# Kernel optimization log

Hardware: AMD Instinct MI355X
Metric: run time of the kernel (lower is better)

Reference implementation:

```python
import jax, jax.numpy as jnp
import numpy as np

# static module hyperparameters (match init_kwargs)
DIMS = 1024
HEAD = 16
HD = DIMS // HEAD          # 64
MAX_ITER = 3
MIN_SIZE = 64
MAX_SIZE = 2048
UP_WIN, DOWN_WIN = 1.1, 0.9
UP_DIFF, DOWN_DIFF = 0.05, 0.001
B, T = 2, 1024


def _ln(x, w, eps=1e-5):
    # torch LayerNorm with bias=False (weight only), biased variance
    m = jnp.mean(x, axis=-1, keepdims=True)
    v = jnp.var(x, axis=-1, keepdims=True)
    return (x - m) * jax.lax.rsqrt(v + eps) * w


def setup_inputs() -> dict:
    key = jax.random.key(0)
    ks = jax.random.split(key, 12)

    def lin_w(k, o, i):
        return (jax.random.normal(k, (o, i), dtype=jnp.float32) / np.sqrt(i)).astype(jnp.float32)

    return {
        "x": jax.random.normal(ks[0], (B, T, DIMS), dtype=jnp.float32),
        "Wq": lin_w(ks[1], DIMS, DIMS), "bq": jnp.zeros((DIMS,), jnp.float32),
        "Wk": lin_w(ks[2], DIMS, DIMS),
        "Wv": lin_w(ks[3], DIMS, DIMS), "bv": jnp.zeros((DIMS,), jnp.float32),
        "Wo": lin_w(ks[4], DIMS, DIMS), "bo": jnp.zeros((DIMS,), jnp.float32),
        "lna_w": jnp.ones((DIMS,), jnp.float32),
        "lnb_w": jnp.ones((DIMS,), jnp.float32),
        "lnc_w": jnp.ones((HD,), jnp.float32),
        "lnd_w": jnp.ones((HD,), jnp.float32),
        "lq_w": lin_w(ks[5], HD, HD), "lq_b": jnp.zeros((HD,), jnp.float32),
        "lk_w": lin_w(ks[6], HD, HD), "lk_b": jnp.zeros((HD,), jnp.float32),
        "lv_w": lin_w(ks[7], HD, HD), "lv_b": jnp.zeros((HD,), jnp.float32),
        "threshold": jnp.float32(0.01),
        "temp_base": jnp.float32(1.0),
        "factor": jnp.float32(0.1),
    }


def _focus(x, Wq, bq, Wk, Wv, bv, Wo, bo, lna_w, lnb_w, lnc_w, lnd_w,
           lq_w, lq_b, lk_w, lk_b, lv_w, lv_b, threshold, temp_base, factor):
    b, t, d = x.shape
    q = _ln(x, lna_w) @ Wq.T + bq
    kk = _ln(x, lnb_w) @ Wk.T
    v = _ln(x, lnb_w) @ Wv.T + bv
    sc = HD ** (-0.25)

    def _shape(u):
        return u.reshape(b, t, HEAD, HD).transpose(0, 2, 1, 3)  # [B,H,T,hd]

    q_full = _shape(q * sc)
    k_full = _shape(kk * sc)
    v_full = _shape(v)

    # .item() calls in torch detach these from the graph
    thr = jax.lax.stop_gradient(threshold)
    fac = jax.lax.stop_gradient(factor)
    t0 = jax.lax.stop_gradient(temp_base)

    cw0 = jnp.int32(max(min(t, MAX_SIZE), MIN_SIZE))
    inv_sqrt_e = jnp.float32(1.0 / np.sqrt(HD))  # SDPA default scale
    pos = jnp.arange(t)

    def step(carry, i):
        qcur, prev, attn, cw, temp, done = carry
        # LocalOut projections over full length (out-of-window part masked below)
        qp = qcur @ lq_w.T + lq_b
        kp = k_full @ lk_w.T + lk_b
        vp = v_full @ lv_w.T + lv_b
        sq = _ln(qp, lnc_w)
        sk = _ln(kp, lnd_w)
        tscale = jnp.where(temp > 0, jax.lax.rsqrt(temp), jnp.float32(1.0))
        sq = sq * tscale
        scores = jnp.einsum('bhqd,bhkd->bhqk', sq, sk) * inv_sqrt_e
        in_win = pos < cw
        scores = jnp.where(in_win[None, None, None, :], scores, -jnp.inf)
        probs = jax.nn.softmax(scores, axis=-1)
        out = jnp.einsum('bhqk,bhkd->bhqd', probs, vp)
        # rows >= cur_win stay zero (iter_out buffer semantics)
        iter_out = jnp.where(in_win[None, None, :, None], out, 0.0)

        diff = jnp.mean(jnp.abs(iter_out - prev))
        converged = (diff < thr + fac * diff) & (i > 0)
        upd = (~done) & (~converged)            # continue iterating
        new_done = done | converged

        attn_n = jnp.where(done, attn, iter_out)
        prev_n = jnp.where(upd, iter_out, prev)
        qcur_n = jnp.where(upd, qcur + iter_out, qcur)
        # _next_win
        up = (cw.astype(jnp.float32) * UP_WIN).astype(jnp.int32)
        down = (cw.astype(jnp.float32) * DOWN_WIN).astype(jnp.int32)
        nw = jnp.where(diff > UP_DIFF, up,
                       jnp.where((diff < DOWN_DIFF) & (cw > MIN_SIZE), down, cw))
        nw = jnp.clip(nw, MIN_SIZE, t)
        cw_n = jnp.where(upd, nw, cw)
        temp_n = jnp.where(upd, temp + jnp.float32(0.005), temp)
        return (qcur_n, prev_n, attn_n, cw_n, temp_n, new_done), None

    zeros = jnp.zeros_like(q_full)
    carry0 = (q_full, zeros, zeros, cw0, t0, jnp.array(False))
    (_, _, attn_out, _, _, _), _ = jax.lax.scan(step, carry0, jnp.arange(MAX_ITER))

    output = attn_out.transpose(0, 2, 1, 3).reshape(b, t, d)
    return output @ Wo.T + bo


def reference(x, Wq, bq, Wk, Wv, bv, Wo, bo, lna_w, lnb_w, lnc_w, lnd_w,
              lq_w, lq_b, lk_w, lk_b, lv_w, lv_b, threshold, temp_base, factor):
    return _focus(x, Wq, bq, Wk, Wv, bv, Wo, bo, lna_w, lnb_w, lnc_w, lnd_w,
                  lq_w, lq_b, lk_w, lk_b, lv_w, lv_b, threshold, temp_base, factor)
```

## Files before the change

### kernel.cpp

```cpp
#include <hip/hip_runtime.h>
#include <hip/hip_bf16.h>

#define BDIM 2
#define TDIM 1024
#define DDIM 1024
#define HDIM 16
#define HD   64
#define RROWS (BDIM * TDIM)
#define BH    (BDIM * HDIM)
#define NHE   (BH * TDIM * HD)
#define NHE4  (NHE / 4)
#define DIFF_BLOCKS 512
#define L2E 1.4426950408889634f

typedef __attribute__((ext_vector_type(8))) short short8v;
typedef __attribute__((ext_vector_type(4))) short short4v;
typedef __attribute__((ext_vector_type(8))) _Float16 half8v;
typedef __attribute__((ext_vector_type(4))) _Float16 half4v;
typedef __attribute__((ext_vector_type(4))) float f32x4;

struct FState {
  int   cw;
  float temp;
  int   done;
  int   upd;
  int   done_prev;
  float thr;
  float fac;
  int   pad;
};

static __device__ __forceinline__ unsigned short f2bf(float x) {
  __hip_bfloat16 h = __float2bfloat16(x);
  return __builtin_bit_cast(unsigned short, h);
}
static __device__ __forceinline__ void gload16(const void* g, void* l) {
  __builtin_amdgcn_global_load_lds(
      (const __attribute__((address_space(1))) void*)g,
      (__attribute__((address_space(3))) void*)l, 16, 0, 0);
}

__global__ void init_kernel(FState* st, const float* thr, const float* tb, const float* fac) {
  if (threadIdx.x == 0 && blockIdx.x == 0) {
    st->cw = TDIM;
    st->temp = tb[0];
    st->done = 0;
    st->done_prev = 0;
    st->upd = 1;
    st->thr = thr[0];
    st->fac = fac[0];
  }
}

__global__ __launch_bounds__(256) void ln_x_kernel(
    const float* __restrict__ x, const float* __restrict__ wa, const float* __restrict__ wb,
    _Float16* __restrict__ xaH, _Float16* __restrict__ xbH)
{
  const int row = blockIdx.x;
  const int tid = threadIdx.x;
  const float4 v = reinterpret_cast<const float4*>(x + (size_t)row * DDIM)[tid];
  float s = v.x + v.y + v.z + v.w;
  float q = v.x * v.x + v.y * v.y + v.z * v.z + v.w * v.w;
#pragma unroll
  for (int off = 1; off < 64; off <<= 1) {
    s += __shfl_xor(s, off);
    q += __shfl_xor(q, off);
  }
  __shared__ float ss[4], qq[4];
  const int lane = tid & 63, wv = tid >> 6;
  if (lane == 0) { ss[wv] = s; qq[wv] = q; }
  __syncthreads();
  s = ss[0] + ss[1] + ss[2] + ss[3];
  q = qq[0] + qq[1] + qq[2] + qq[3];
  const float mean = s * (1.0f / DDIM);
  const float var  = q * (1.0f / DDIM) - mean * mean;
  const float inv  = rsqrtf(var + 1e-5f);
  const float4 a4 = reinterpret_cast<const float4*>(wa)[tid];
  const float4 b4 = reinterpret_cast<const float4*>(wb)[tid];
  const float hv[4] = { (v.x - mean) * inv, (v.y - mean) * inv,
                        (v.z - mean) * inv, (v.w - mean) * inv };
  const float av[4] = { a4.x, a4.y, a4.z, a4.w };
  const float bv[4] = { b4.x, b4.y, b4.z, b4.w };
  half4v ha, hb;
#pragma unroll
  for (int j = 0; j < 4; ++j) {
    ha[j] = (_Float16)(hv[j] * av[j]);
    hb[j] = (_Float16)(hv[j] * bv[j]);
  }
  *reinterpret_cast<half4v*>(xaH + (size_t)row * DDIM + tid * 4) = ha;
  *reinterpret_cast<half4v*>(xbH + (size_t)row * DDIM + tid * 4) = hb;
}

__global__ __launch_bounds__(256) void w_cvt_kernel(
    const float* __restrict__ W0, const float* __restrict__ W1,
    const float* __restrict__ W2, const float* __restrict__ W3,
    const float* __restrict__ W4,
    _Float16* __restrict__ O0, _Float16* __restrict__ O1,
    _Float16* __restrict__ O2, _Float16* __restrict__ O3,
    _Float16* __restrict__ O4)
{
  const float* W; _Float16* O;
  switch (blockIdx.y) {
    case 0:  W = W0; O = O0; break;
    case 1:  W = W1; O = O1; break;
    case 2:  W = W2; O = O2; break;
    case 3:  W = W3; O = O3; break;
    default:
      if (blockIdx.x >= 4) return;
      W = W4; O = O4; break;
  }
  const int r = blockIdx.x;
  const int tid = threadIdx.x;
  const float4 v = reinterpret_cast<const float4*>(W + (size_t)r * 1024)[tid];
  half4v h;
  h[0] = (_Float16)v.x; h[1] = (_Float16)v.y;
  h[2] = (_Float16)v.z; h[3] = (_Float16)v.w;
  *reinterpret_cast<half4v*>(O + (size_t)r * 1024 + tid * 4) = h;
}

template<int CMODE>
__global__ __launch_bounds__(256) void gemm_mfma_kernel(
    const _Float16* __restrict__ A0, const _Float16* __restrict__ W0,
    const float* __restrict__ b0, float* __restrict__ C0, float s0,
    const _Float16* __restrict__ A1, const _Float16* __restrict__ W1,
    const float* __restrict__ b1, float* __restrict__ C1, float s1,
    const _Float16* __restrict__ A2, const _Float16* __restrict__ W2,
    const float* __restrict__ b2, float* __restrict__ C2, float s2)
{
  const _Float16* A; const _Float16* W; const float* bias; float* C; float scale;
  switch (blockIdx.z) {
    case 0:  A = A0; W = W0; bias = b0; C = C0; scale = s0; break;
    case 1:  A = A1; W = W1; bias = b1; C = C1; scale = s1; break;
    default: A = A2; W = W2; bias = b2; C = C2; scale = s2; break;
  }
  __shared__ __align__(16) _Float16 As[128 * 32];
  __shared__ __align__(16) _Float16 Ws[128 * 32];
  const int tid = threadIdx.x;
  const int wv = tid >> 6, lane = tid & 63;
  const int wm = wv >> 1, wn = wv & 1;
  const int bm = blockIdx.x;
  const int bn = blockIdx.y;

  const _Float16* gA[2]; const _Float16* gW[2];
  _Float16* lA[2]; _Float16* lW[2];
#pragma unroll
  for (int j = 0; j < 2; ++j) {
    const int chunk = wv * 2 + j;
    const int r = chunk * 16 + (lane >> 2);
    const int ce = (lane & 3) * 8;
    gA[j] = A + (size_t)(bm * 128 + r) * 1024 + ce;
    gW[j] = W + (size_t)(bn * 128 + r) * 1024 + ce;
    lA[j] = As + chunk * 512;
    lW[j] = Ws + chunk * 512;
  }

  f32x4 acc[4][4] = {};
  const int rb = lane & 15;
  const int kb = (lane >> 4) * 8;

  for (int ks = 0; ks < 1024; ks += 32) {
    __syncthreads();
#pragma unroll
    for (int j = 0; j < 2; ++j) {
      gload16(gA[j] + ks, lA[j]);
      gload16(gW[j] + ks, lW[j]);
    }
    __syncthreads();
    half8v af[4], wf[4];
#pragma unroll
    for (int f = 0; f < 4; ++f) {
      af[f] = *reinterpret_cast<const half8v*>(As + (wm * 64 + f * 16 + rb) * 32 + kb);
      wf[f] = *reinterpret_cast<const half8v*>(Ws + (wn * 64 + f * 16 + rb) * 32 + kb);
    }
#pragma unroll
    for (int i = 0; i < 4; ++i)
#pragma unroll
      for (int j2 = 0; j2 < 4; ++j2)
        acc[i][j2] = __builtin_amdgcn_mfma_f32_16x16x32_f16(af[i], wf[j2], acc[i][j2], 0, 0, 0);
  }

#pragma unroll
  for (int j2 = 0; j2 < 4; ++j2) {
    const int n = bn * 128 + wn * 64 + j2 * 16 + (lane & 15);
    const float bv_ = bias ? bias[n] : 0.0f;
#pragma unroll
    for (int i = 0; i < 4; ++i) {
#pragma unroll
      for (int r = 0; r < 4; ++r) {
        const int m = bm * 128 + wm * 64 + i * 16 + (lane >> 4) * 4 + r;
        const float v = (acc[i][j2][r] + bv_) * scale;
        size_t ci;
        if constexpr (CMODE == 0) {
          ci = (size_t)m * 1024 + n;
        } else {
          const int b = m >> 10, t = m & (TDIM - 1);
          ci = ((size_t)(b * HDIM + (n >> 6)) * TDIM + t) * HD + (n & 63);
        }
        C[ci] = v;
      }
    }
  }
}

template<int OUT_MODE, bool DO_LN>
static __device__ __forceinline__ void headproj_body(
    const float* __restrict__ in, unsigned short* __restrict__ out,
    const float* __restrict__ w, const float* __restrict__ bias,
    const float* __restrict__ lnw, float* wl, unsigned short* tT)
{
  const int tid = threadIdx.x;
  for (int idx = tid; idx < 4096; idx += 256) {
    const int d = idx >> 6, i = idx & 63;
    wl[i * 65 + d] = w[idx];
  }
  const int lane = tid & 63, wv = tid >> 6;
  const float bd = bias[lane];
  float lw = 1.0f;
  if constexpr (DO_LN) lw = lnw[lane];
  __syncthreads();
  const int rowBase = blockIdx.x * 32 + wv * 8;
  for (int rr = 0; rr < 8; ++rr) {
    const int row = rowBase + rr;
    const float h = in[(size_t)row * HD + lane];
    float y = bd;
#pragma unroll
    for (int i = 0; i < 64; ++i) {
      const float hv = __uint_as_float((unsigned)__builtin_amdgcn_readlane((int)__float_as_uint(h), i));
      y += wl[i * 65 + lane] * hv;
    }
    if constexpr (DO_LN) {
      float s = y;
#pragma unroll
      for (int off = 1; off < 64; off <<= 1) s += __shfl_xor(s, off);
      const float mean = s * (1.0f / 64.0f);
      const float t0 = y - mean;
      float v2 = t0 * t0;
#pragma unroll
      for (int off = 1; off < 64; off <<= 1) v2 += __shfl_xor(v2, off);
      y = t0 * rsqrtf(v2 * (1.0f / 64.0f) + 1e-5f) * lw;
    }
    if constexpr (OUT_MODE == 0) {
      out[(size_t)row * HD + lane] = f2bf(y);
    } else {
      tT[lane * 34 + wv * 8 + rr] = f2bf(y);
    }
  }
  if constexpr (OUT_MODE == 1) {
    __syncthreads();
    const int hd = tid >> 2, tseg = (tid & 3) * 8;
    const int r0 = blockIdx.x * 32;
    const int bh = r0 >> 10, t0 = r0 & (TDIM - 1);
    short8v v;
#pragma unroll
    for (int i = 0; i < 8; ++i) v[i] = (short)tT[hd * 34 + tseg + i];
    *reinterpret_cast<short8v*>(out + ((size_t)bh * HD + hd) * TDIM + t0 + tseg) = v;
  }
}

__global__ __launch_bounds__(256) void headproj_kv_kernel(
    const float* __restrict__ kin, unsigned short* __restrict__ skb,
    const float* __restrict__ lkw, const float* __restrict__ lkb,
    const float* __restrict__ lnd,
    const float* __restrict__ vin, unsigned short* __restrict__ vpT,
    const float* __restrict__ lvw, const float* __restrict__ lvb)
{
  __shared__ float wl[64 * 65];
  __shared__ unsigned short tT[64 * 34];
  if (blockIdx.y == 0)
    headproj_body<0, true >(kin, skb, lkw, lkb, lnd, wl, tT);
  else
    headproj_body<1, false>(vin, vpT, lvw, lvb, (const float*)nullptr, wl, tT);
}

__global__ __launch_bounds__(512) void attn_mfma_kernel(
    const float* __restrict__ qcur, const unsigned short* __restrict__ sk,
    const unsigned short* __restrict__ vpT, float* __restrict__ io,
    const float* __restrict__ prev, _Float16* __restrict__ attnH,
    const _Float16* __restrict__ lqwH, const float* __restrict__ lqb,
    const float* __restrict__ lnc, float* __restrict__ partials,
    const FState* __restrict__ st, int is_first)
{
  if (st->done) return;
  const int lid = blockIdx.x;
  const int xcd = lid & 7;
  const int rr_ = lid >> 3;
  const int qb  = rr_ & 15;
  const int bh  = (rr_ >> 4) * 8 + xcd;

  const int cw = st->cw;
  const int tid = threadIdx.x;
  const int wv = tid >> 6, lane = tid & 63;
  const int wq = wv & 3, wk = wv >> 2;
  const int ql = lane & 15, hi = lane >> 4;
  const int qbase = qb * 64 + wq * 16;
  const int q = qbase + ql;
  const size_t baseRow = (size_t)bh * TDIM * HD;
  const size_t baseT   = (size_t)bh * HD * TDIM;
  float* orow = io + baseRow + (size_t)q * HD;
  const float* prow = prev + baseRow + (size_t)q * HD;
  float* qcrow = const_cast<float*>(qcur) + baseRow + (size_t)q * HD;
  const bool wvalid = (qbase < cw);
  _Float16* arow = attnH + (size_t)((bh >> 4) * TDIM + q) * 1024 + (bh & 15) * HD;

  __shared__ __align__(16) unsigned char KV[2][2][2][8192];
  __shared__ __align__(16) unsigned char PJ[8][2048];
  float* wred = reinterpret_cast<float*>(&KV[1][1][0][0]);

  const int sub  = lane >> 3;
  const int colB = (lane & 7) * 16;
  const int scol = (colB ^ (sub << 4)) >> 1;

  const int kb0 = wk * 512;
  const unsigned short* kSrc0 = sk  + baseRow + (size_t)(kb0 + wq * 16 + sub) * HD + scol;
  const unsigned short* vSrc0 = vpT + baseT  + (size_t)(wq * 16 + sub) * TDIM + scol;

  unsigned char* pj = (unsigned char*)PJ[wv];
  const unsigned swz8 = (unsigned)((ql & 7) << 4);

  const int nch0 = (min(cw, 512) + 63) >> 6;
  const int nch1 = (cw > 512) ? ((cw - 512 + 63) >> 6) : 0;
  const int nchOwn = wk ? nch1 : nch0;

  if (nchOwn > 0) {
#pragma unroll
    for (int jj = 0; jj < 2; ++jj) {
      gload16(kSrc0 + (size_t)(jj * 8) * HD, &KV[wk][0][0][(wq * 2 + jj) * 1024]);
      gload16(vSrc0 + (size_t)(jj * 8) * TDIM + kb0, &KV[wk][0][1][(wq * 2 + jj) * 1024]);
    }
  }

  short8v qf0, qf1;
  if (wvalid) {
    const float tp = st->temp;
    const float ts = (tp > 0.0f ? rsqrtf(tp) : 1.0f) * 0.125f;
    half8v qh0, qh1;
    {
      const f32x4 a0 = *reinterpret_cast<const f32x4*>(qcrow + hi * 8);
      const f32x4 a1 = *reinterpret_cast<const f32x4*>(qcrow + hi * 8 + 4);
      const f32x4 b0 = *reinterpret_cast<const f32x4*>(qcrow + 32 + hi * 8);
      const f32x4 b1 = *reinterpret_cast<const f32x4*>(qcrow + 32 + hi * 8 + 4);
#pragma unroll
      for (int j = 0; j < 4; ++j) {
        qh0[j] = (_Float16)a0[j]; qh0[4 + j] = (_Float16)a1[j];
        qh1[j] = (_Float16)b0[j]; qh1[4 + j] = (_Float16)b1[j];
      }
    }
    f32x4 sp[4];
#pragma unroll
    for (int f = 0; f < 4; ++f) {
      const half8v a0 = *reinterpret_cast<const half8v*>(lqwH + (f * 16 + ql) * 64 + hi * 8);
      const half8v a1 = *reinterpret_cast<const half8v*>(lqwH + (f * 16 + ql) * 64 + 32 + hi * 8);
      f32x4 acc = {};
      acc = __builtin_amdgcn_mfma_f32_16x16x32_f16(a0, qh0, acc, 0, 0, 0);
      acc = __builtin_amdgcn_mfma_f32_16x16x32_f16(a1, qh1, acc, 0, 0, 0);
      sp[f] = acc;
    }
    float sum = 0.f;
#pragma unroll
    for (int f = 0; f < 4; ++f) {
      const f32x4 b4 = *reinterpret_cast<const f32x4*>(lqb + f * 16 + hi * 4);
      sp[f] += b4;
      sum += (sp[f][0] + sp[f][1]) + (sp[f][2] + sp[f][3]);
    }
    sum += __shfl_xor(sum, 16);
    sum += __shfl_xor(sum, 32);
    const float mean = sum * (1.0f / 64.0f);
    float vs = 0.f;
#pragma unroll
    for (int f = 0; f < 4; ++f) {
#pragma unroll
      for (int r = 0; r < 4; ++r) {
        const float t0 = sp[f][r] - mean;
        sp[f][r] = t0;
        vs += t0 * t0;
      }
    }
    vs += __shfl_xor(vs, 16);
    vs += __shfl_xor(vs, 32);
    const float inv = rsqrtf(vs * (1.0f / 64.0f) + 1e-5f);
    const unsigned wb = (unsigned)(ql * 128 + hi * 8);
#pragma unroll
    for (int f = 0; f < 4; ++f) {
      const f32x4 lc = *reinterpret_cast<const f32x4*>(lnc + f * 16 + hi * 4);
      const float y0 = sp[f][0] * inv * lc[0] * ts;
      const float y1 = sp[f][1] * inv * lc[1] * ts;
      const float y2 = sp[f][2] * inv * lc[2] * ts;
      const float y3 = sp[f][3] * inv * lc[3] * ts;
      *reinterpret_cast<unsigned*>(pj + ((wb + f * 32)     ^ swz8)) =
          (unsigned)f2bf(y0) | ((unsigned)f2bf(y1) << 16);
      *reinterpret_cast<unsigned*>(pj + ((wb + f * 32 + 4) ^ swz8)) =
          (unsigned)f2bf(y2) | ((unsigned)f2bf(y3) << 16);
    }
    qf0 = *reinterpret_cast<short8v*>(pj + ((unsigned)(ql * 128 + hi * 16) ^ swz8));
    qf1 = *reinterpret_cast<short8v*>(pj + ((unsigned)(ql * 128 + 64 + hi * 16) ^ swz8));
  }
  __syncthreads();

  float m = -1e30f, l = 0.f;
  f32x4 o[4] = {};
  int cur = 0;
  for (int ch = 0; ch < nch0; ++ch) {
    if (ch + 1 < nchOwn) {
      const size_t kn = (size_t)(ch + 1) * 64;
#pragma unroll
      for (int jj = 0; jj < 2; ++jj) {
        gload16(kSrc0 + (kn + (size_t)(jj * 8)) * HD, &KV[wk][cur ^ 1][0][(wq * 2 + jj) * 1024]);
        gload16(vSrc0 + (size_t)(jj * 8) * TDIM + kb0 + kn, &KV[wk][cur ^ 1][1][(wq * 2 + jj) * 1024]);
      }
    }
    if (wvalid && ch < nchOwn) {
      const int k0 = kb0 + ch * 64;
      const unsigned char* kt = &KV[wk][cur][0][0];
      const unsigned char* vt = &KV[wk][cur][1][0];
      f32x4 s[4];
#pragma unroll
      for (int f = 0; f < 4; ++f) {
        const unsigned rb = (unsigned)((f * 16 + ql) * 128);
        const short8v a0 = *reinterpret_cast<const short8v*>(kt + rb + ((unsigned)(hi * 16) ^ swz8));
        const short8v a1 = *reinterpret_cast<const short8v*>(kt + rb + ((unsigned)(64 + hi * 16) ^ swz8));
        f32x4 acc = {};
        acc = __builtin_amdgcn_mfma_f32_16x16x32_bf16(a0, qf0, acc, 0, 0, 0);
        acc = __builtin_amdgcn_mfma_f32_16x16x32_bf16(a1, qf1, acc, 0, 0, 0);
        s[f] = acc;
      }
      float mc = -1e30f;
      if (k0 + 64 > cw) {
#pragma unroll
        for (int f = 0; f < 4; ++f)
#pragma unroll
          for (int r = 0; r < 4; ++r) {
            float v = s[f][r];
            if (k0 + f * 16 + hi * 4 + r >= cw) v = -1e30f;
            s[f][r] = v;
            mc = fmaxf(mc, v);
          }
      } else {
#pragma unroll
        for (int f = 0; f < 4; ++f)
#pragma unroll
          for (int r = 0; r < 4; ++r) mc = fmaxf(mc, s[f][r]);
      }
      mc = fmaxf(mc, __shfl_xor(mc, 16));
      mc = fmaxf(mc, __shfl_xor(mc, 32));
      if (__any(mc > m + 8.0f)) {
        const float mn = fmaxf(m, mc);
        const float c = __builtin_amdgcn_exp2f((m - mn) * L2E);
        l *= c;
#pragma unroll
        for (int f = 0; f < 4; ++f) o[f] *= c;
        m = mn;
      }
      float ls = 0.f;
      unsigned pk[8];
#pragma unroll
      for (int f = 0; f < 4; ++f) {
        const float p0 = __builtin_amdgcn_exp2f((s[f][0] - m) * L2E);
        const float p1 = __builtin_amdgcn_exp2f((s[f][1] - m) * L2E);
        const float p2 = __builtin_amdgcn_exp2f((s[f][2] - m) * L2E);
        const float p3 = __builtin_amdgcn_exp2f((s[f][3] - m) * L2E);
        ls += (p0 + p1) + (p2 + p3);
        pk[f * 2]     = (unsigned)f2bf(p0) | ((unsigned)f2bf(p1) << 16);
        pk[f * 2 + 1] = (unsigned)f2bf(p2) | ((unsigned)f2bf(p3) << 16);
      }
      ls += __shfl_xor(ls, 16);
      ls += __shfl_xor(ls, 32);
      l += ls;
      const unsigned wb = (unsigned)(ql * 128 + hi * 8);
#pragma unroll
      for (int f = 0; f < 4; ++f) {
        *reinterpret_cast<unsigned*>(pj + ((wb + f * 32)     ^ swz8)) = pk[f * 2];
        *reinterpret_cast<unsigned*>(pj + ((wb + f * 32 + 4) ^ swz8)) = pk[f * 2 + 1];
      }
#pragma unroll
      for (int kh = 0; kh < 2; ++kh) {
        const short8v pb = *reinterpret_cast<short8v*>(
            pj + ((unsigned)(ql * 128 + kh * 64 + hi * 16) ^ swz8));
#pragma unroll
        for (int f = 0; f < 4; ++f) {
          const unsigned rb = (unsigned)((f * 16 + ql) * 128);
          const short8v av = *reinterpret_cast<const short8v*>(
              vt + rb + ((unsigned)(kh * 64 + hi * 16) ^ swz8));
          o[f] = __builtin_amdgcn_mfma_f32_16x16x32_bf16(av, pb, o[f], 0, 0, 0);
        }
      }
    }
    __syncthreads();
    cur ^= 1;
  }

  float* Obuf = reinterpret_cast<float*>(&KV[0][0][0][0]);
  if (wk == 1 && wvalid) {
    if (hi == 0) {
      Obuf[4352 + wq * 16 + ql] = m;
      Obuf[4416 + wq * 16 + ql] = l;
    }
#pragma unroll
    for (int f = 0; f < 4; ++f)
      *reinterpret_cast<f32x4*>(&Obuf[(wq * 16 + ql) * 68 + f * 16 + hi * 4]) = o[f];
  }
  __syncthreads();

  float pd = 0.0f;
  if (wk == 0) {
    if (wvalid) {
      const float m1 = Obuf[4352 + wq * 16 + ql];
      const float l1 = Obuf[4416 + wq * 16 + ql];
      const float mn = fmaxf(m, m1);
      const float c0 = __builtin_amdgcn_exp2f((m - mn) * L2E);
      const float c1 = __builtin_amdgcn_exp2f((m1 - mn) * L2E);
      const float lt = l * c0 + l1 * c1;
      const bool valid = (q < cw);
      const float invl = valid ? (1.0f / lt) : 0.0f;
#pragma unroll
      for (int f = 0; f < 4; ++f) {
        const f32x4 o1 = *reinterpret_cast<const f32x4*>(&Obuf[(wq * 16 + ql) * 68 + f * 16 + hi * 4]);
        const f32x4 vo = (o[f] * c0 + o1 * c1) * invl;
        *reinterpret_cast<f32x4*>(orow + f * 16 + hi * 4) = vo;
        half4v h4;
        h4[0] = (_Float16)vo[0]; h4[1] = (_Float16)vo[1];
        h4[2] = (_Float16)vo[2]; h4[3] = (_Float16)vo[3];
        *reinterpret_cast<half4v*>(arow + f * 16 + hi * 4) = h4;
        const f32x4 qv = *reinterpret_cast<const f32x4*>(qcrow + f * 16 + hi * 4);
        *reinterpret_cast<f32x4*>(qcrow + f * 16 + hi * 4) = qv + vo;
        if (!is_first) {
          const f32x4 pv = *reinterpret_cast<const f32x4*>(prow + f * 16 + hi * 4);
          pd += fabsf(vo[0] - pv[0]) + fabsf(vo[1] - pv[1]) +
                fabsf(vo[2] - pv[2]) + fabsf(vo[3] - pv[3]);
        } else {
          pd += fabsf(vo[0]) + fabsf(vo[1]) + fabsf(vo[2]) + fabsf(vo[3]);
        }
      }
    } else {
      const f32x4 z = {0.f, 0.f, 0.f, 0.f};
      const half4v hz = { (_Float16)0.f, (_Float16)0.f, (_Float16)0.f, (_Float16)0.f };
#pragma unroll
      for (int f = 0; f < 4; ++f) {
        *reinterpret_cast<f32x4*>(orow + f * 16 + hi * 4) = z;
        *reinterpret_cast<half4v*>(arow + f * 16 + hi * 4) = hz;
        if (!is_first) {
          const f32x4 pv = *reinterpret_cast<const f32x4*>(prow + f * 16 + hi * 4);
          pd += fabsf(pv[0]) + fabsf(pv[1]) + fabsf(pv[2]) + fabsf(pv[3]);
        }
      }
    }
  }

#pragma unroll
  for (int off = 1; off < 64; off <<= 1) pd += __shfl_xor(pd, off);
  if (lane == 0) wred[wv] = pd;
  __syncthreads();
  if (tid == 0)
    partials[lid] = wred[0] + wred[1] + wred[2] + wred[3] +
                    wred[4] + wred[5] + wred[6] + wred[7];
}

__global__ __launch_bounds__(256) void state_update_kernel(
    FState* __restrict__ st, const float* __restrict__ partials, int iter)
{
  const int tid = threadIdx.x;
  float s = 0.0f;
  for (int i = tid; i < DIFF_BLOCKS; i += 256) s += partials[i];
  __shared__ float red[256];
  red[tid] = s;
  __syncthreads();
  for (int off = 128; off > 0; off >>= 1) {
    if (tid < off) red[tid] += red[tid + off];
    __syncthreads();
  }
  if (tid == 0) {
    const int done_prev = st->done;
    st->done_prev = done_prev;
    if (!done_prev) {
      const float diff = red[0] * (1.0f / (float)NHE);
      const bool conv = (diff < st->thr + st->fac * diff) && (iter > 0);
      st->upd  = conv ? 0 : 1;
      st->done = conv ? 1 : 0;
      if (!conv) {
        const int cw = st->cw;
        const int up = (int)((float)cw * 1.1f);
        const int dn = (int)((float)cw * 0.9f);
        int nw = (diff > 0.05f) ? up : ((diff < 0.001f && cw > 64) ? dn : cw);
        nw = nw < 64 ? 64 : (nw > TDIM ? TDIM : nw);
        st->cw = nw;
        st->temp += 0.005f;
      }
    } else {
      st->upd = 0;
    }
  }
}

extern "C" void kernel_launch(void* const* d_in, const int* in_sizes, int n_in,
                              void* d_out, int out_size, void* d_ws, size_t ws_size,
                              hipStream_t stream)
{
  const float* x   = (const float*)d_in[0];
  const float* Wq  = (const float*)d_in[1];
  const float* bq  = (const float*)d_in[2];
  const float* Wk  = (const float*)d_in[3];
  const float* Wv  = (const float*)d_in[4];
  const float* bv  = (const float*)d_in[5];
  const float* Wo  = (const float*)d_in[6];
  const float* bo  = (const float*)d_in[7];
  const float* lna = (const float*)d_in[8];
  const float* lnb = (const float*)d_in[9];
  const float* lnc = (const float*)d_in[10];
  const float* lnd = (const float*)d_in[11];
  const float* lqw = (const float*)d_in[12];
  const float* lqb = (const float*)d_in[13];
  const float* lkw = (const float*)d_in[14];
  const float* lkb = (const float*)d_in[15];
  const float* lvw = (const float*)d_in[16];
  const float* lvb = (const float*)d_in[17];
  const float* thr = (const float*)d_in[18];
  const float* tb  = (const float*)d_in[19];
  const float* fac = (const float*)d_in[20];
  float* out = (float*)d_out;

  float* f0   = (float*)d_ws;
  float* qcur = f0;
  float* io0  = f0 + (size_t)NHE;
  float* io1  = f0 + 2 * (size_t)NHE;
  _Float16* h0   = (_Float16*)(f0 + 3 * (size_t)NHE);
  _Float16* xaH  = h0;
  _Float16* attnH = h0;
  _Float16* xbH  = h0 + (size_t)RROWS * 1024;
  _Float16* WqH  = xbH + (size_t)RROWS * 1024;
  _Float16* WkH  = WqH + (size_t)1048576;
  _Float16* WvH  = WkH + (size_t)1048576;
  _Float16* WoH  = WvH + (size_t)1048576;
  _Float16* lqwH = WoH + (size_t)1048576;
  unsigned short* skb = (unsigned short*)(lqwH + 4096);
  unsigned short* vpT = skb + (size_t)NHE;
  float* partials = (float*)(vpT + (size_t)NHE);
  FState* st = (FState*)(partials + DIFF_BLOCKS);

  constexpr float SC = 0.35355339059327379f;

  hipLaunchKernelGGL(init_kernel, dim3(1), dim3(64), 0, stream, st, thr, tb, fac);
  hipLaunchKernelGGL(ln_x_kernel, dim3(RROWS), dim3(256), 0, stream, x, lna, lnb, xaH, xbH);
  hipLaunchKernelGGL(w_cvt_kernel, dim3(1024, 5), dim3(256), 0, stream,
                     Wq, Wk, Wv, Wo, lqw, WqH, WkH, WvH, WoH, lqwH);

  hipLaunchKernelGGL((gemm_mfma_kernel<1>), dim3(16, 8, 3), dim3(256), 0, stream,
                     xaH, WqH, bq, qcur, SC,
                     xbH, WkH, (const float*)nullptr, io0, SC,
                     xbH, WvH, bv, io1, 1.0f);

  hipLaunchKernelGGL(headproj_kv_kernel, dim3(1024, 2), dim3(256), 0, stream,
                     io0, skb, lkw, lkb, lnd, io1, vpT, lvw, lvb);

  for (int it = 0; it < 3; ++it) {
    float* io   = (it & 1) ? io1 : io0;
    float* prev = (it & 1) ? io0 : io1;
    hipLaunchKernelGGL(attn_mfma_kernel, dim3(DIFF_BLOCKS), dim3(512), 0, stream,
                       qcur, skb, vpT, io, prev, attnH, lqwH, lqb, lnc,
                       partials, st, it == 0 ? 1 : 0);
    hipLaunchKernelGGL(state_update_kernel, dim3(1), dim3(256), 0, stream,
                       st, partials, it);
  }

  hipLaunchKernelGGL((gemm_mfma_kernel<0>), dim3(16, 8, 1), dim3(256), 0, stream,
                     attnH, WoH, bo, out, 1.0f,
                     attnH, WoH, bo, out, 1.0f,
                     attnH, WoH, bo, out, 1.0f);
}
```

Before: 161.3 us.

## Merge init, layernorm and weight-convert kernels; add MFMA priority hints

Folds the state-init, input layernorm and weight fp32-to-fp16 conversion kernels into a single prep kernel dispatched over a flat block range, removing two kernel launches. It also raises wave priority with s_setprio around the QK and PV MFMA sections of the attention kernel, and unrolls the partials reduction in the state-update kernel to a fixed two loads per thread. The merged grid puts branch divergence by block index into one kernel, and the priority hints may or may not help wave scheduling.

```diff
diff --git a/kernel.cpp b/kernel.cpp
--- a/kernel.cpp
+++ b/kernel.cpp
@@ -40,24 +40,56 @@
       (__attribute__((address_space(3))) void*)l, 16, 0, 0);
 }
 
-__global__ void init_kernel(FState* st, const float* thr, const float* tb, const float* fac) {
-  if (threadIdx.x == 0 && blockIdx.x == 0) {
-    st->cw = TDIM;
-    st->temp = tb[0];
-    st->done = 0;
-    st->done_prev = 0;
-    st->upd = 1;
-    st->thr = thr[0];
-    st->fac = fac[0];
-  }
-}
-
-__global__ __launch_bounds__(256) void ln_x_kernel(
+__global__ __launch_bounds__(256) void prep_kernel(
     const float* __restrict__ x, const float* __restrict__ wa, const float* __restrict__ wb,
-    _Float16* __restrict__ xaH, _Float16* __restrict__ xbH)
+    _Float16* __restrict__ xaH, _Float16* __restrict__ xbH,
+    const float* __restrict__ W0, const float* __restrict__ W1,
+    const float* __restrict__ W2, const float* __restrict__ W3,
+    const float* __restrict__ W4,
+    _Float16* __restrict__ O0, _Float16* __restrict__ O1,
+    _Float16* __restrict__ O2, _Float16* __restrict__ O3,
+    _Float16* __restrict__ O4,
+    FState* st, const float* thr, const float* tb, const float* fac)
 {
-  const int row = blockIdx.x;
+  const int bid = blockIdx.x;
   const int tid = threadIdx.x;
+
+  if (bid >= 6148) {
+    if (tid == 0) {
+      st->cw = TDIM;
+      st->temp = tb[0];
+      st->done = 0;
+      st->done_prev = 0;
+      st->upd = 1;
+      st->thr = thr[0];
+      st->fac = fac[0];
+    }
+    return;
+  }
+
+  if (bid >= 2048) {
+    const int idx = bid - 2048;
+    const float* W; _Float16* O; int r;
+    if (bid >= 6144) { W = W4; O = O4; r = bid - 6144; }
+    else {
+      const int mat = idx >> 10;
+      r = idx & 1023;
+      switch (mat) {
+        case 0:  W = W0; O = O0; break;
+        case 1:  W = W1; O = O1; break;
+        case 2:  W = W2; O = O2; break;
+        default: W = W3; O = O3; break;
+      }
+    }
+    const float4 v = reinterpret_cast<const float4*>(W + (size_t)r * 1024)[tid];
+    half4v h;
+    h[0] = (_Float16)v.x; h[1] = (_Float16)v.y;
+    h[2] = (_Float16)v.z; h[3] = (_Float16)v.w;
+    *reinterpret_cast<half4v*>(O + (size_t)r * 1024 + tid * 4) = h;
+    return;
+  }
+
+  const int row = bid;
   const float4 v = reinterpret_cast<const float4*>(x + (size_t)row * DDIM)[tid];
   float s = v.x + v.y + v.z + v.w;
   float q = v.x * v.x + v.y * v.y + v.z * v.z + v.w * v.w;
@@ -91,33 +123,6 @@
   *reinterpret_cast<half4v*>(xbH + (size_t)row * DDIM + tid * 4) = hb;
 }
 
-__global__ __launch_bounds__(256) void w_cvt_kernel(
-    const float* __restrict__ W0, const float* __restrict__ W1,
-    const float* __restrict__ W2, const float* __restrict__ W3,
-    const float* __restrict__ W4,
-    _Float16* __restrict__ O0, _Float16* __restrict__ O1,
-    _Float16* __restrict__ O2, _Float16* __restrict__ O3,
-    _Float16* __restrict__ O4)
-{
-  const float* W; _Float16* O;
-  switch (blockIdx.y) {
-    case 0:  W = W0; O = O0; break;
-    case 1:  W = W1; O = O1; break;
-    case 2:  W = W2; O = O2; break;
-    case 3:  W = W3; O = O3; break;
-    default:
-      if (blockIdx.x >= 4) return;
-      W = W4; O = O4; break;
-  }
-  const int r = blockIdx.x;
-  const int tid = threadIdx.x;
-  const float4 v = reinterpret_cast<const float4*>(W + (size_t)r * 1024)[tid];
-  half4v h;
-  h[0] = (_Float16)v.x; h[1] = (_Float16)v.y;
-  h[2] = (_Float16)v.z; h[3] = (_Float16)v.w;
-  *reinterpret_cast<half4v*>(O + (size_t)r * 1024 + tid * 4) = h;
-}
-
 template<int CMODE>
 __global__ __launch_bounds__(256) void gemm_mfma_kernel(
     const _Float16* __restrict__ A0, const _Float16* __restrict__ W0,
@@ -413,6 +418,7 @@
       const unsigned char* kt = &KV[wk][cur][0][0];
       const unsigned char* vt = &KV[wk][cur][1][0];
       f32x4 s[4];
+      __builtin_amdgcn_s_setprio(1);
 #pragma unroll
       for (int f = 0; f < 4; ++f) {
         const unsigned rb = (unsigned)((f * 16 + ql) * 128);
@@ -423,6 +429,7 @@
         acc = __builtin_amdgcn_mfma_f32_16x16x32_bf16(a1, qf1, acc, 0, 0, 0);
         s[f] = acc;
       }
+      __builtin_amdgcn_s_setprio(0);
       float mc = -1e30f;
       if (k0 + 64 > cw) {
 #pragma unroll
@@ -471,6 +478,7 @@
         *reinterpret_cast<unsigned*>(pj + ((wb + f * 32)     ^ swz8)) = pk[f * 2];
         *reinterpret_cast<unsigned*>(pj + ((wb + f * 32 + 4) ^ swz8)) = pk[f * 2 + 1];
       }
+      __builtin_amdgcn_s_setprio(1);
 #pragma unroll
       for (int kh = 0; kh < 2; ++kh) {
         const short8v pb = *reinterpret_cast<short8v*>(
@@ -483,6 +491,7 @@
           o[f] = __builtin_amdgcn_mfma_f32_16x16x32_bf16(av, pb, o[f], 0, 0, 0);
         }
       }
+      __builtin_amdgcn_s_setprio(0);
     }
     __syncthreads();
     cur ^= 1;
@@ -558,8 +567,7 @@
     FState* __restrict__ st, const float* __restrict__ partials, int iter)
 {
   const int tid = threadIdx.x;
-  float s = 0.0f;
-  for (int i = tid; i < DIFF_BLOCKS; i += 256) s += partials[i];
+  float s = partials[tid] + partials[tid + 256];
   __shared__ float red[256];
   red[tid] = s;
   __syncthreads();
@@ -637,10 +645,10 @@
 
   constexpr float SC = 0.35355339059327379f;
 
-  hipLaunchKernelGGL(init_kernel, dim3(1), dim3(64), 0, stream, st, thr, tb, fac);
-  hipLaunchKernelGGL(ln_x_kernel, dim3(RROWS), dim3(256), 0, stream, x, lna, lnb, xaH, xbH);
-  hipLaunchKernelGGL(w_cvt_kernel, dim3(1024, 5), dim3(256), 0, stream,
-                     Wq, Wk, Wv, Wo, lqw, WqH, WkH, WvH, WoH, lqwH);
+  hipLaunchKernelGGL(prep_kernel, dim3(6149), dim3(256), 0, stream,
+                     x, lna, lnb, xaH, xbH,
+                     Wq, Wk, Wv, Wo, lqw, WqH, WkH, WvH, WoH, lqwH,
+                     st, thr, tb, fac);
 
   hipLaunchKernelGGL((gemm_mfma_kernel<1>), dim3(16, 8, 3), dim3(256), 0, stream,
                      xaH, WqH, bq, qcur, SC,
```

Result: faster. 154.4 us (median of 2 runs) (-4.3%).
